# Optimization experiments

Measured on AMD Instinct MI355X. Metric: run time of the kernel, lower is better.

## Reference

```python
import jax, jax.numpy as jnp
import numpy as np

B, T, D, H = 4, 2048, 1024, 16
HD = D // H  # head dim = 64


def setup_inputs() -> dict:
    key = jax.random.key(0)
    ks = jax.random.split(key, 12)
    s = 1.0 / np.sqrt(D)
    inp = {
        "Q": jax.random.normal(ks[0], (B, T, D), jnp.float32),
        "K": jax.random.normal(ks[1], (B, T, D), jnp.float32),
        "V": jax.random.normal(ks[2], (B, T, D), jnp.float32),
        "mask": jnp.tril(jnp.ones((T, T), jnp.int32))[None, None],  # causal [1,1,T,T]
        "Wq": jax.random.normal(ks[3], (D, D), jnp.float32) * s,
        "bq": jax.random.normal(ks[4], (D,), jnp.float32) * s,
        "Wk": jax.random.normal(ks[5], (D, D), jnp.float32) * s,
        "bk": jax.random.normal(ks[6], (D,), jnp.float32) * s,
        "Wv": jax.random.normal(ks[7], (D, D), jnp.float32) * s,
        "bv": jax.random.normal(ks[8], (D,), jnp.float32) * s,
        "Wo": jax.random.normal(ks[9], (D, D), jnp.float32) * s,
        "bo": jax.random.normal(ks[10], (D,), jnp.float32) * s,
    }
    return inp


def reference(Q, K, V, mask, Wq, bq, Wk, bk, Wv, bv, Wo, bo):
    b, t, d = Q.shape
    # projections (torch Linear: x @ W^T + b)
    q = (Q @ Wq.T + bq).reshape(b, t, H, HD).transpose(0, 2, 1, 3)  # [b,h,t,hd]
    k = (K @ Wk.T + bk).reshape(b, t, H, HD).transpose(0, 2, 1, 3)
    v = (V @ Wv.T + bv).reshape(b, t, H, HD).transpose(0, 2, 1, 3)
    score = jnp.einsum("bhqd,bhkd->bhqk", q, k) / jnp.sqrt(jnp.float32(HD))
    score = jnp.where(mask == 0, jnp.float32(-1e9), score)
    attn = jax.nn.softmax(score, axis=-1)
    out = jnp.einsum("bhqk,bhkd->bhqd", attn, v)
    out = out.transpose(0, 2, 1, 3).reshape(b, t, d)
    return out @ Wo.T + bo
```

## Files before the change

### kernel.cpp

```cpp
#include <hip/hip_runtime.h>
#include <stdint.h>

#define B_SZ  4
#define T_SEQ 2048
#define DIM   1024
#define NH    16
#define HD    64
#define M_TOT (B_SZ * T_SEQ)

typedef unsigned short u16;
typedef unsigned long long u64;
typedef __attribute__((ext_vector_type(8))) __bf16 bf16x8;
typedef __attribute__((ext_vector_type(4))) float  floatx4;
typedef __attribute__((ext_vector_type(16))) float floatx16;

#define SCL_Q (0.125f * 1.44269504089f)

__device__ __forceinline__ u16 f2bf(float f) {
  union { float f; uint32_t u; } v; v.f = f;
  uint32_t r = v.u + 0x7fffu + ((v.u >> 16) & 1u);
  return (u16)(r >> 16);
}

__device__ __forceinline__ void gl_lds16(const void* g, void* l) {
  __builtin_amdgcn_global_load_lds(
      (const __attribute__((address_space(1))) uint32_t*)g,
      (__attribute__((address_space(3))) uint32_t*)l, 16, 0, 0);
}

__global__ __launch_bounds__(256) void cvt_all(
    const float* __restrict__ s0, const float* __restrict__ s1,
    const float* __restrict__ s2, const float* __restrict__ s3,
    const float* __restrict__ s4, const float* __restrict__ s5,
    const float* __restrict__ s6,
    u16* __restrict__ d0, u16* __restrict__ d1, u16* __restrict__ d2,
    u16* __restrict__ d3, u16* __restrict__ d4, u16* __restrict__ d5,
    u16* __restrict__ d6) {
  const float* s; u16* d; int n;
  switch (blockIdx.y) {
    case 0: s = s0; d = d0; n = DIM * DIM; break;
    case 1: s = s1; d = d1; n = DIM * DIM; break;
    case 2: s = s2; d = d2; n = DIM * DIM; break;
    case 3: s = s3; d = d3; n = DIM * DIM; break;
    case 4: s = s4; d = d4; n = M_TOT * DIM; break;
    case 5: s = s5; d = d5; n = M_TOT * DIM; break;
    default: s = s6; d = d6; n = M_TOT * DIM; break;
  }
  int i = (blockIdx.x * 256 + threadIdx.x) * 8;
  if (i >= n) return;
  float4 a = *(const float4*)(s + i);
  float4 b = *(const float4*)(s + i + 4);
  uint4 o;
  o.x = (uint32_t)f2bf(a.x) | ((uint32_t)f2bf(a.y) << 16);
  o.y = (uint32_t)f2bf(a.z) | ((uint32_t)f2bf(a.w) << 16);
  o.z = (uint32_t)f2bf(b.x) | ((uint32_t)f2bf(b.y) << 16);
  o.w = (uint32_t)f2bf(b.z) | ((uint32_t)f2bf(b.w) << 16);
  *(uint4*)(d + i) = o;
}

#define BKG 64
__global__ __launch_bounds__(256) void gemm_qkv(
    const u16* __restrict__ Qb, const u16* __restrict__ Kb,
    const u16* __restrict__ Vb,
    const u16* __restrict__ Wq, const u16* __restrict__ Wk,
    const u16* __restrict__ Wv,
    const float* __restrict__ bq, const float* __restrict__ bk,
    const float* __restrict__ bv,
    u16* __restrict__ qo, u16* __restrict__ ko, u16* __restrict__ vo) {
  const u16* A; const u16* Bw; const float* bias; u16* Co;
  if (blockIdx.z == 0)      { A = Qb; Bw = Wq; bias = bq; Co = qo; }
  else if (blockIdx.z == 1) { A = Kb; Bw = Wk; bias = bk; Co = ko; }
  else                      { A = Vb; Bw = Wv; bias = bv; Co = vo; }

  __shared__ u16 As[128 * 64];
  __shared__ u16 Bs[128 * 64];

  const int tid  = threadIdx.x;
  const int wave = tid >> 6, lane = tid & 63;
  const int quad = lane >> 4, l16 = lane & 15;
  const int wm = wave >> 1, wn = wave & 1;
  const int m0 = blockIdx.x * 128, n0 = blockIdx.y * 128;

  const floatx4 FZ = {0.f, 0.f, 0.f, 0.f};
  floatx4 acc[4][4];
#pragma unroll
  for (int mt = 0; mt < 4; ++mt)
#pragma unroll
    for (int nt = 0; nt < 4; ++nt) acc[mt][nt] = FZ;

  for (int k0 = 0; k0 < DIM; k0 += BKG) {
    __syncthreads();
#pragma unroll
    for (int j = 0; j < 4; ++j) {
      int pc = j * 256 + tid;
      int r = pc >> 3, c = pc & 7;
      int sc = c ^ (r & 7);
      gl_lds16(A  + (size_t)(m0 + r) * DIM + k0 + sc * 8,
               &As[(j * 256 + wave * 64) * 8]);
      gl_lds16(Bw + (size_t)(n0 + r) * DIM + k0 + sc * 8,
               &Bs[(j * 256 + wave * 64) * 8]);
    }
    __syncthreads();

#pragma unroll
    for (int kk = 0; kk < 2; ++kk) {
      bf16x8 af[4], bfr[4];
#pragma unroll
      for (int mt = 0; mt < 4; ++mt) {
        int ra = wm * 64 + mt * 16 + l16;
        af[mt] = *(const bf16x8*)&As[ra * 64 + (((kk * 4 + quad) ^ (ra & 7)) * 8)];
      }
#pragma unroll
      for (int nt = 0; nt < 4; ++nt) {
        int rb = wn * 64 + nt * 16 + l16;
        bfr[nt] = *(const bf16x8*)&Bs[rb * 64 + (((kk * 4 + quad) ^ (rb & 7)) * 8)];
      }
#pragma unroll
      for (int mt = 0; mt < 4; ++mt)
#pragma unroll
        for (int nt = 0; nt < 4; ++nt)
          acc[mt][nt] = __builtin_amdgcn_mfma_f32_16x16x32_bf16(
              af[mt], bfr[nt], acc[mt][nt], 0, 0, 0);
    }
  }

  if (blockIdx.z == 2) {
#pragma unroll
    for (int nt = 0; nt < 4; ++nt) {
      int n = n0 + wn * 64 + nt * 16 + l16;
      float bb = bias[n];
      int h = n >> 6, hd = n & 63;
#pragma unroll
      for (int mt = 0; mt < 4; ++mt) {
        int mbase = m0 + wm * 64 + mt * 16 + quad * 4;
        int b = mbase >> 11, t = mbase & (T_SEQ - 1);
        u64 pk = 0;
#pragma unroll
        for (int r = 0; r < 4; ++r)
          pk |= (u64)f2bf(acc[mt][nt][r] + bb) << (16 * r);
        *(u64*)&Co[((size_t)((b * NH + h) * HD + hd)) * T_SEQ + t] = pk;
      }
    }
  } else {
    const float sc = (blockIdx.z == 0) ? SCL_Q : 1.0f;
#pragma unroll
    for (int nt = 0; nt < 4; ++nt) {
      int n = n0 + wn * 64 + nt * 16 + l16;
      float bb = bias[n];
      int h = n >> 6, hd = n & 63;
#pragma unroll
      for (int mt = 0; mt < 4; ++mt) {
#pragma unroll
        for (int r = 0; r < 4; ++r) {
          int m = m0 + wm * 64 + mt * 16 + quad * 4 + r;
          int b = m >> 11, t = m & (T_SEQ - 1);
          Co[((size_t)(b * NH + h) * T_SEQ + t) * HD + hd] =
              f2bf((acc[mt][nt][r] + bb) * sc);
        }
      }
    }
  }
}

__global__ __launch_bounds__(256) void flash_attn(
    const u16* __restrict__ qp, const u16* __restrict__ kp,
    const u16* __restrict__ vp, u16* __restrict__ ao) {
  const int bh = blockIdx.x;
  const int qt = (T_SEQ / 128 - 1) - blockIdx.y;
  const int b = bh >> 4, h = bh & 15;
  const u16* Qg = qp + (size_t)bh * T_SEQ * HD;
  const u16* Kg = kp + (size_t)bh * T_SEQ * HD;
  const u16* Vg = vp + (size_t)bh * HD * T_SEQ;

  __shared__ u16 lds[4][64 * 64];

  const int tid = threadIdx.x, wave = tid >> 6, lane = tid & 63;
  const int hi = lane >> 5, c31 = lane & 31;
  const int lr8 = lane >> 3, lc8 = lane & 7;

  const int qrow = qt * 128 + wave * 32 + c31;

  bf16x8 bq[4];
#pragma unroll
  for (int cth = 0; cth < 4; ++cth)
    bq[cth] = *(const bf16x8*)(Qg + (size_t)qrow * HD + cth * 16 + hi * 8);

  floatx16 o0, o1;
#pragma unroll
  for (int i = 0; i < 16; ++i) { o0[i] = 0.f; o1[i] = 0.f; }
  float l_p = 0.f;

  int koff[4];
#pragma unroll
  for (int x = 0; x < 4; ++x)
    koff[x] = c31 * 64 + (((x * 2 + hi) ^ (c31 & 7)) * 8);

#pragma unroll
  for (int i = 0; i < 2; ++i) {
    int r = i * 32 + wave * 8 + lr8;
    int sc = lc8 ^ (r & 7);
    gl_lds16(Kg + (size_t)r * HD + sc * 8, &lds[0][(i * 32 + wave * 8) * 64]);
    gl_lds16(Vg + (size_t)r * T_SEQ + sc * 8, &lds[1][(i * 32 + wave * 8) * 64]);
  }

  const int nkb = 2 * qt + 2;
  const int qwmin = qt * 128 + wave * 32;
  const int qwmax = qwmin + 31;
  int p = 0;
  for (int kb = 0; kb < nkb; ++kb) {
    __syncthreads();
    if (kb + 1 < nkb) {
      const u16* Kgk = Kg + (size_t)(kb + 1) * 64 * HD;
      const u16* Vgk = Vg + (size_t)(kb + 1) * 64;
#pragma unroll
      for (int i = 0; i < 2; ++i) {
        int r = i * 32 + wave * 8 + lr8;
        int sc = lc8 ^ (r & 7);
        gl_lds16(Kgk + (size_t)r * HD + sc * 8,
                 &lds[(p ^ 1) * 2][(i * 32 + wave * 8) * 64]);
        gl_lds16(Vgk + (size_t)r * T_SEQ + sc * 8,
                 &lds[(p ^ 1) * 2 + 1][(i * 32 + wave * 8) * 64]);
      }
    }

    if (kb * 64 <= qwmax) {
      const u16* Ks = &lds[p * 2][0];
      const u16* Vs = &lds[p * 2 + 1][0];

      floatx16 s0, s1;
#pragma unroll
      for (int i = 0; i < 16; ++i) { s0[i] = 0.f; s1[i] = 0.f; }
#pragma unroll
      for (int cth = 0; cth < 4; ++cth) {
        bf16x8 ka = *(const bf16x8*)&Ks[koff[cth]];
        bf16x8 kb2 = *(const bf16x8*)&Ks[koff[cth] + 32 * 64];
        s0 = __builtin_amdgcn_mfma_f32_32x32x16_bf16(ka, bq[cth], s0, 0, 0, 0);
        s1 = __builtin_amdgcn_mfma_f32_32x32x16_bf16(kb2, bq[cth], s1, 0, 0, 0);
      }

      if (kb * 64 + 63 > qwmin) {
        int kvb = kb * 64 + 4 * hi;
#pragma unroll
        for (int r = 0; r < 16; ++r) {
          int kvr = kvb + (r & 3) + 8 * (r >> 2);
          if (kvr > qrow)      s0[r] = -3e38f;
          if (kvr + 32 > qrow) s1[r] = -3e38f;
        }
      }

      uint32_t pk0[8], pk1[8];
      float rs = 0.f;
#pragma unroll
      for (int rr = 0; rr < 8; ++rr) {
        union { float f; uint32_t u; } x0, x1, y0, y1;
        x0.f = __builtin_amdgcn_exp2f(s0[2 * rr]);
        x1.f = __builtin_amdgcn_exp2f(s0[2 * rr + 1]);
        y0.f = __builtin_amdgcn_exp2f(s1[2 * rr]);
        y1.f = __builtin_amdgcn_exp2f(s1[2 * rr + 1]);
        rs += (x0.f + x1.f) + (y0.f + y1.f);
        pk0[rr] = __builtin_amdgcn_perm(x1.u, x0.u, 0x07060302);
        pk1[rr] = __builtin_amdgcn_perm(y1.u, y0.u, 0x07060302);
      }
      l_p += rs;

#pragma unroll
      for (int cc = 0; cc < 4; ++cc) {
        const uint32_t* pks = (cc & 2) ? pk1 : pk0;
        const int e4 = (cc & 1) * 4;
        auto r0 = __builtin_amdgcn_permlane32_swap(pks[e4 + 0], pks[e4 + 2],
                                                   false, false);
        auto r1 = __builtin_amdgcn_permlane32_swap(pks[e4 + 1], pks[e4 + 3],
                                                   false, false);
        union { uint32_t u[4]; bf16x8 v; } bp;
        bp.u[0] = r0[0]; bp.u[1] = r1[0]; bp.u[2] = r0[1]; bp.u[3] = r1[1];
        bf16x8 va = *(const bf16x8*)&Vs[koff[cc]];
        bf16x8 vb = *(const bf16x8*)&Vs[koff[cc] + 32 * 64];
        o0 = __builtin_amdgcn_mfma_f32_32x32x16_bf16(va, bp.v, o0, 0, 0, 0);
        o1 = __builtin_amdgcn_mfma_f32_32x32x16_bf16(vb, bp.v, o1, 0, 0, 0);
      }
    }
    p ^= 1;
  }

  {
    float l = l_p + __shfl_xor(l_p, 32);
    float inv = 1.0f / l;
    const size_t obase = (size_t)(b * T_SEQ + qrow) * DIM + h * HD;
#pragma unroll
    for (int u4 = 0; u4 < 4; ++u4) {
      u64 w0 = 0, w1 = 0;
#pragma unroll
      for (int r = 0; r < 4; ++r) {
        w0 |= (u64)f2bf(o0[4 * u4 + r] * inv) << (16 * r);
        w1 |= (u64)f2bf(o1[4 * u4 + r] * inv) << (16 * r);
      }
      *(u64*)&ao[obase + 8 * u4 + 4 * hi] = w0;
      *(u64*)&ao[obase + 32 + 8 * u4 + 4 * hi] = w1;
    }
  }
}

__global__ __launch_bounds__(256) void gemm_out(
    const u16* __restrict__ Ain, const u16* __restrict__ Wo,
    const float* __restrict__ bo, float* __restrict__ out) {
  __shared__ u16 As[128 * 64];
  __shared__ u16 Bs[128 * 64];

  const int tid  = threadIdx.x;
  const int wave = tid >> 6, lane = tid & 63;
  const int quad = lane >> 4, l16 = lane & 15;
  const int wm = wave >> 1, wn = wave & 1;
  const int m0 = blockIdx.x * 128, n0 = blockIdx.y * 128;

  const floatx4 FZ = {0.f, 0.f, 0.f, 0.f};
  floatx4 acc[4][4];
#pragma unroll
  for (int mt = 0; mt < 4; ++mt)
#pragma unroll
    for (int nt = 0; nt < 4; ++nt) acc[mt][nt] = FZ;

  for (int k0 = 0; k0 < DIM; k0 += BKG) {
    __syncthreads();
#pragma unroll
    for (int j = 0; j < 4; ++j) {
      int pc = j * 256 + tid;
      int r = pc >> 3, c = pc & 7;
      int sc = c ^ (r & 7);
      gl_lds16(Ain + (size_t)(m0 + r) * DIM + k0 + sc * 8,
               &As[(j * 256 + wave * 64) * 8]);
      gl_lds16(Wo  + (size_t)(n0 + r) * DIM + k0 + sc * 8,
               &Bs[(j * 256 + wave * 64) * 8]);
    }
    __syncthreads();

#pragma unroll
    for (int kk = 0; kk < 2; ++kk) {
      bf16x8 af[4], bfr[4];
#pragma unroll
      for (int mt = 0; mt < 4; ++mt) {
        int ra = wm * 64 + mt * 16 + l16;
        af[mt] = *(const bf16x8*)&As[ra * 64 + (((kk * 4 + quad) ^ (ra & 7)) * 8)];
      }
#pragma unroll
      for (int nt = 0; nt < 4; ++nt) {
        int rb = wn * 64 + nt * 16 + l16;
        bfr[nt] = *(const bf16x8*)&Bs[rb * 64 + (((kk * 4 + quad) ^ (rb & 7)) * 8)];
      }
#pragma unroll
      for (int mt = 0; mt < 4; ++mt)
#pragma unroll
        for (int nt = 0; nt < 4; ++nt)
          acc[mt][nt] = __builtin_amdgcn_mfma_f32_16x16x32_bf16(
              af[mt], bfr[nt], acc[mt][nt], 0, 0, 0);
    }
  }

#pragma unroll
  for (int nt = 0; nt < 4; ++nt) {
    int n = n0 + wn * 64 + nt * 16 + l16;
    float bb = bo[n];
#pragma unroll
    for (int mt = 0; mt < 4; ++mt)
#pragma unroll
      for (int r = 0; r < 4; ++r) {
        int m = m0 + wm * 64 + mt * 16 + quad * 4 + r;
        out[(size_t)m * DIM + n] = acc[mt][nt][r] + bb;
      }
  }
}

extern "C" void kernel_launch(void* const* d_in, const int* in_sizes, int n_in,
                              void* d_out, int out_size, void* d_ws,
                              size_t ws_size, hipStream_t stream) {
  const float* Q  = (const float*)d_in[0];
  const float* K  = (const float*)d_in[1];
  const float* V  = (const float*)d_in[2];
  const float* Wq = (const float*)d_in[4];
  const float* bq = (const float*)d_in[5];
  const float* Wk = (const float*)d_in[6];
  const float* bk = (const float*)d_in[7];
  const float* Wv = (const float*)d_in[8];
  const float* bv = (const float*)d_in[9];
  const float* Wo = (const float*)d_in[10];
  const float* bo = (const float*)d_in[11];
  float* out = (float*)d_out;

  u16* wqb = (u16*)d_ws;
  u16* wkb = wqb + 1048576;
  u16* wvb = wkb + 1048576;
  u16* wob = wvb + 1048576;
  u16* Qb  = wob + 1048576;
  u16* Kb  = Qb + (size_t)M_TOT * DIM;
  u16* Vb  = Kb + (size_t)M_TOT * DIM;
  u16* qp  = Vb + (size_t)M_TOT * DIM;
  u16* kp  = qp + (size_t)M_TOT * DIM;
  u16* vp  = kp + (size_t)M_TOT * DIM;
  u16* aop = vp + (size_t)M_TOT * DIM;

  cvt_all<<<dim3(M_TOT * DIM / 2048, 7), 256, 0, stream>>>(
      Wq, Wk, Wv, Wo, Q, K, V, wqb, wkb, wvb, wob, Qb, Kb, Vb);

  gemm_qkv<<<dim3(M_TOT / 128, DIM / 128, 3), 256, 0, stream>>>(
      Qb, Kb, Vb, wqb, wkb, wvb, bq, bk, bv, qp, kp, vp);

  flash_attn<<<dim3(B_SZ * NH, T_SEQ / 128), 256, 0, stream>>>(qp, kp, vp, aop);

  gemm_out<<<dim3(M_TOT / 128, DIM / 128), 256, 0, stream>>>(aop, wob, bo, out);
}
```

Measured before the change: 316.7 us.

## Enlarge flash-attention blocks to 256 queries with triple-buffered K/V prefetch

Flash attention now runs 512-thread blocks covering 256 query rows, so each K/V tile loaded into LDS is shared by eight waves instead of four. K/V loads move from double to triple buffering, prefetching two tiles ahead and waiting with explicit vmcnt counts rather than a full __syncthreads. The query-tile order is remapped to interleave long and short causal blocks for load balance. In exchange, blocks are half as many and use more LDS, and correctness relies on the hand-written waitcnt accounting.

```diff
diff --git a/kernel.cpp b/kernel.cpp
--- a/kernel.cpp
+++ b/kernel.cpp
@@ -162,29 +162,41 @@
   }
 }
 
-__global__ __launch_bounds__(256) void flash_attn(
+__global__ __launch_bounds__(512, 2) void flash_attn(
     const u16* __restrict__ qp, const u16* __restrict__ kp,
     const u16* __restrict__ vp, u16* __restrict__ ao) {
   const int bh = blockIdx.x;
-  const int qt = (T_SEQ / 128 - 1) - blockIdx.y;
+  const int y = blockIdx.y;
+  const int qt = (y < 4) ? (7 - y) : (y - 4);
   const int b = bh >> 4, h = bh & 15;
   const u16* Qg = qp + (size_t)bh * T_SEQ * HD;
   const u16* Kg = kp + (size_t)bh * T_SEQ * HD;
   const u16* Vg = vp + (size_t)bh * HD * T_SEQ;
 
-  __shared__ u16 lds[4][64 * 64];
+  __shared__ u16 lds[6][64 * 64];
 
   const int tid = threadIdx.x, wave = tid >> 6, lane = tid & 63;
   const int hi = lane >> 5, c31 = lane & 31;
   const int lr8 = lane >> 3, lc8 = lane & 7;
 
-  const int qrow = qt * 128 + wave * 32 + c31;
+  const int qrow = qt * 256 + wave * 32 + c31;
 
   bf16x8 bq[4];
 #pragma unroll
   for (int cth = 0; cth < 4; ++cth)
     bq[cth] = *(const bf16x8*)(Qg + (size_t)qrow * HD + cth * 16 + hi * 8);
 
+  const int nkb = 4 * qt + 4;
+  const int srow = wave * 8 + lr8;
+  const int ssc = lc8 ^ (srow & 7);
+
+  gl_lds16(Kg + (size_t)srow * HD + ssc * 8, &lds[0][wave * 8 * 64]);
+  gl_lds16(Vg + (size_t)srow * T_SEQ + ssc * 8, &lds[1][wave * 8 * 64]);
+  gl_lds16(Kg + (size_t)(64 + srow) * HD + ssc * 8, &lds[2][wave * 8 * 64]);
+  gl_lds16(Vg + (size_t)srow * T_SEQ + 64 + ssc * 8, &lds[3][wave * 8 * 64]);
+
+  asm volatile("" :: "v"(bq[0]), "v"(bq[1]), "v"(bq[2]), "v"(bq[3]));
+
   floatx16 o0, o1;
 #pragma unroll
   for (int i = 0; i < 16; ++i) { o0[i] = 0.f; o1[i] = 0.f; }
@@ -195,37 +207,28 @@
   for (int x = 0; x < 4; ++x)
     koff[x] = c31 * 64 + (((x * 2 + hi) ^ (c31 & 7)) * 8);
 
-#pragma unroll
-  for (int i = 0; i < 2; ++i) {
-    int r = i * 32 + wave * 8 + lr8;
-    int sc = lc8 ^ (r & 7);
-    gl_lds16(Kg + (size_t)r * HD + sc * 8, &lds[0][(i * 32 + wave * 8) * 64]);
-    gl_lds16(Vg + (size_t)r * T_SEQ + sc * 8, &lds[1][(i * 32 + wave * 8) * 64]);
-  }
-
-  const int nkb = 2 * qt + 2;
-  const int qwmin = qt * 128 + wave * 32;
+  const int qwmin = qt * 256 + wave * 32;
   const int qwmax = qwmin + 31;
-  int p = 0;
+  int pc_ = 0;
+  int ps_ = 2;
   for (int kb = 0; kb < nkb; ++kb) {
-    __syncthreads();
-    if (kb + 1 < nkb) {
-      const u16* Kgk = Kg + (size_t)(kb + 1) * 64 * HD;
-      const u16* Vgk = Vg + (size_t)(kb + 1) * 64;
-#pragma unroll
-      for (int i = 0; i < 2; ++i) {
-        int r = i * 32 + wave * 8 + lr8;
-        int sc = lc8 ^ (r & 7);
-        gl_lds16(Kgk + (size_t)r * HD + sc * 8,
-                 &lds[(p ^ 1) * 2][(i * 32 + wave * 8) * 64]);
-        gl_lds16(Vgk + (size_t)r * T_SEQ + sc * 8,
-                 &lds[(p ^ 1) * 2 + 1][(i * 32 + wave * 8) * 64]);
-      }
+    if (kb + 1 < nkb) asm volatile("s_waitcnt vmcnt(2)" ::: "memory");
+    else              asm volatile("s_waitcnt vmcnt(0)" ::: "memory");
+    __builtin_amdgcn_s_barrier();
+    __builtin_amdgcn_sched_barrier(0);
+
+    if (kb + 2 < nkb) {
+      const u16* Kgk = Kg + (size_t)(kb + 2) * 64 * HD;
+      const u16* Vgk = Vg + (size_t)(kb + 2) * 64;
+      gl_lds16(Kgk + (size_t)srow * HD + ssc * 8, &lds[ps_ * 2][wave * 8 * 64]);
+      gl_lds16(Vgk + (size_t)srow * T_SEQ + ssc * 8,
+               &lds[ps_ * 2 + 1][wave * 8 * 64]);
+      ps_ = (ps_ == 2) ? 0 : ps_ + 1;
     }
 
     if (kb * 64 <= qwmax) {
-      const u16* Ks = &lds[p * 2][0];
-      const u16* Vs = &lds[p * 2 + 1][0];
+      const u16* Ks = &lds[pc_ * 2][0];
+      const u16* Vs = &lds[pc_ * 2 + 1][0];
 
       floatx16 s0, s1;
 #pragma unroll
@@ -279,7 +282,7 @@
         o1 = __builtin_amdgcn_mfma_f32_32x32x16_bf16(vb, bp.v, o1, 0, 0, 0);
       }
     }
-    p ^= 1;
+    pc_ = (pc_ == 2) ? 0 : pc_ + 1;
   }
 
   {
@@ -403,7 +406,7 @@
   gemm_qkv<<<dim3(M_TOT / 128, DIM / 128, 3), 256, 0, stream>>>(
       Qb, Kb, Vb, wqb, wkb, wvb, bq, bk, bv, qp, kp, vp);
 
-  flash_attn<<<dim3(B_SZ * NH, T_SEQ / 128), 256, 0, stream>>>(qp, kp, vp, aop);
+  flash_attn<<<dim3(B_SZ * NH, T_SEQ / 256), 512, 0, stream>>>(qp, kp, vp, aop);
 
   gemm_out<<<dim3(M_TOT / 128, DIM / 128), 256, 0, stream>>>(aop, wob, bo, out);
 }
```

Result: faster. 309.2 us (-2.4%).
